# Optimization experiments

Hardware: AMD Instinct MI355X
Metric: run time of the kernel (lower is better)

## Reference

```python
import jax, jax.numpy as jnp
import numpy as np

BLOCK = 16
FP4_LEVELS = jnp.array([0.0, 0.5, 1.0, 1.5, 2.0, 3.0, 4.0, 6.0], dtype=jnp.float32)
FP4_MIDS = jnp.array([0.25, 0.75, 1.25, 1.75, 2.5, 3.5, 5.0], dtype=jnp.float32)
E4M3_MAX = 448.0
FP4_MAX = 6.0


def _fp4_round(v):
    # round-to-nearest onto signed E2M1 grid {0,.5,1,1.5,2,3,4,6}
    a = jnp.minimum(jnp.abs(v), FP4_MAX)
    idx = jnp.searchsorted(FP4_MIDS, a, side='right')
    return jnp.sign(v) * FP4_LEVELS[idx]


def _encode_scale(block_amax, global_amax):
    # two-level NVFP4 scaling: block scale stored as FP8 E4M3 relative to global scale
    g_scale = global_amax / (E4M3_MAX * FP4_MAX)
    s = block_amax / FP4_MAX
    s_q = jnp.clip(s / g_scale, 0.0, E4M3_MAX).astype(jnp.float8_e4m3fn).astype(jnp.float32) * g_scale
    return s_q


def nvfp4_qdq_1d(x, block=BLOCK):
    # blockwise fake-quant along the last dim (activations)
    sh = x.shape
    xb = x.reshape(sh[:-1] + (sh[-1] // block, block))
    g_amax = jnp.max(jnp.abs(x))
    b_amax = jnp.max(jnp.abs(xb), axis=-1, keepdims=True)
    s = _encode_scale(b_amax, g_amax)
    s_safe = jnp.where(s > 0, s, 1.0)
    dq = _fp4_round(xb / s_safe) * s
    return dq.reshape(sh)


def nvfp4_qdq_2d(w, block=BLOCK):
    # (16,16) 2D block fake-quant for the weight [out, in]
    O, I = w.shape
    wb = w.reshape(O // block, block, I // block, block)
    g_amax = jnp.max(jnp.abs(w))
    b_amax = jnp.max(jnp.abs(wb), axis=(1, 3), keepdims=True)
    s = _encode_scale(b_amax, g_amax)
    s_safe = jnp.where(s > 0, s, 1.0)
    dq = _fp4_round(wb / s_safe) * s
    return dq.reshape(O, I)


def setup_inputs() -> dict:
    key = jax.random.key(0)
    kx, kw = jax.random.split(key)
    B, S, D_IN, D_OUT = 4, 2048, 4096, 4096
    x = jax.random.normal(kx, (B, S, D_IN), dtype=jnp.float32)
    weight = jax.random.normal(kw, (D_OUT, D_IN), dtype=jnp.float32) * 0.02
    bias = jnp.zeros((D_OUT,), dtype=jnp.float32)
    return {"x": x, "weight": weight, "bias": bias}


def reference(x, weight, bias):
    x_hat = nvfp4_qdq_1d(x)
    x_ste = x + jax.lax.stop_gradient(x_hat - x)
    w_hat = nvfp4_qdq_2d(weight)
    w_ste = weight + jax.lax.stop_gradient(w_hat - weight)
    y = jnp.einsum('bsi,oi->bso', x_ste, w_ste)
    return y + bias
```

## Files before the change

### kernel.cpp

```cpp
#include <hip/hip_runtime.h>

typedef unsigned short u16;
typedef unsigned int u32;
typedef __bf16 bf16x8 __attribute__((ext_vector_type(8)));
typedef float f32x4 __attribute__((ext_vector_type(4)));


__device__ __forceinline__ float e4m3_rne(float r) {
  if (r < 0.015625f) {
    return rintf(r * 512.0f) * (1.0f / 512.0f);
  }
  u32 u = __float_as_uint(r);
  u32 lsb = (u >> 20) & 1u;
  u += 0x7FFFFu + lsb;
  u &= 0xFFF00000u;
  return __uint_as_float(u);
}

__device__ __forceinline__ float fp4_level(float a, const float* t) {
  return a < t[3] ? (a < t[1] ? (a < t[0] ? 0.0f : 0.5f)
                              : (a < t[2] ? 1.0f : 1.5f))
                  : (a < t[5] ? (a < t[4] ? 2.0f : 3.0f)
                              : (a < t[6] ? 4.0f : 6.0f));
}

__device__ __forceinline__ void gload_lds16(const u16* g, void* l) {
  __builtin_amdgcn_global_load_lds(
      (const __attribute__((address_space(1))) void*)g,
      (__attribute__((address_space(3))) void*)l, 16, 0, 0);
}


__global__ void __launch_bounds__(256) amax_part_kernel(const float4* __restrict__ p,
                                                        int n4, float* __restrict__ part) {
  float m = 0.0f;
  int stride = gridDim.x * 256;
  for (int i = blockIdx.x * 256 + threadIdx.x; i < n4; i += stride) {
    float4 v = p[i];
    m = fmaxf(m, fmaxf(fmaxf(fabsf(v.x), fabsf(v.y)), fmaxf(fabsf(v.z), fabsf(v.w))));
  }
#pragma unroll
  for (int o = 32; o > 0; o >>= 1) m = fmaxf(m, __shfl_xor(m, o));
  __shared__ float red[4];
  int wid = threadIdx.x >> 6, lane = threadIdx.x & 63;
  if (lane == 0) red[wid] = m;
  __syncthreads();
  if (threadIdx.x == 0)
    part[blockIdx.x] = fmaxf(fmaxf(red[0], red[1]), fmaxf(red[2], red[3]));
}

__global__ void __launch_bounds__(256) finalize_kernel(const float* __restrict__ px,
                                                       const float* __restrict__ pw,
                                                       float* __restrict__ scal,
                                                       int nx, int nw) {
  int tid = threadIdx.x;
  float mx = 0.0f, mw = 0.0f;
  for (int i = tid; i < nx; i += 256) mx = fmaxf(mx, px[i]);
  for (int i = tid; i < nw; i += 256) mw = fmaxf(mw, pw[i]);
#pragma unroll
  for (int o = 32; o > 0; o >>= 1) {
    mx = fmaxf(mx, __shfl_xor(mx, o));
    mw = fmaxf(mw, __shfl_xor(mw, o));
  }
  __shared__ float rx[4], rw[4];
  int wid = tid >> 6, lane = tid & 63;
  if (lane == 0) { rx[wid] = mx; rw[wid] = mw; }
  __syncthreads();
  if (tid == 0) {
    scal[0] = fmaxf(fmaxf(rx[0], rx[1]), fmaxf(rx[2], rx[3]));
    scal[1] = fmaxf(fmaxf(rw[0], rw[1]), fmaxf(rw[2], rw[3]));
  }
}


__global__ void __launch_bounds__(256) quant_x_kernel(const float* __restrict__ x,
                                                      const float* __restrict__ scal,
                                                      u16* __restrict__ q, int nblk) {
  int b = blockIdx.x * 256 + threadIdx.x;
  if (b >= nblk) return;
  const float4* px = (const float4*)(x + (size_t)b * 16);
  float4 v[4];
  v[0] = px[0]; v[1] = px[1]; v[2] = px[2]; v[3] = px[3];
  float am = 0.0f;
  const float* vf = (const float*)v;
#pragma unroll
  for (int i = 0; i < 16; ++i) am = fmaxf(am, fabsf(vf[i]));

  float g = scal[0] / 2688.0f;
  float ratio = fminf(fmaxf((am / 6.0f) / g, 0.0f), 448.0f);
  float sq = e4m3_rne(ratio);
  float s = sq * g;
  float ss = s > 0.0f ? s : 1.0f;
  float t[7] = {0.25f * ss, 0.75f * ss, 1.25f * ss, 1.75f * ss,
                2.5f * ss, 3.5f * ss, 5.0f * ss};

  union { u16 h[16]; uint4 v4[2]; } ou;
#pragma unroll
  for (int i = 0; i < 16; ++i) {
    float qv = copysignf(fp4_level(fabsf(vf[i]), t) * sq, vf[i]);
    ou.h[i] = (u16)(__float_as_uint(qv) >> 16);
  }
  uint4* qd = (uint4*)(q + (size_t)b * 16);
  qd[0] = ou.v4[0];
  qd[1] = ou.v4[1];
}


__global__ void __launch_bounds__(256) quant_w_kernel(const float* __restrict__ w,
                                                      const float* __restrict__ scal,
                                                      u16* __restrict__ q, int ntc, int K) {
  int wav = blockIdx.x * 4 + (threadIdx.x >> 6);
  int lane = threadIdx.x & 63;
  int tr = wav / ntc, tc = wav % ntc;
  int r = lane >> 2, c = (lane & 3) * 4;
  size_t off = (size_t)(tr * 16 + r) * K + tc * 16 + c;
  float4 v = *(const float4*)(w + off);
  float am = fmaxf(fmaxf(fabsf(v.x), fabsf(v.y)), fmaxf(fabsf(v.z), fabsf(v.w)));
#pragma unroll
  for (int o = 32; o > 0; o >>= 1) am = fmaxf(am, __shfl_xor(am, o));

  float g = scal[1] / 2688.0f;
  float ratio = fminf(fmaxf((am / 6.0f) / g, 0.0f), 448.0f);
  float sq = e4m3_rne(ratio);
  float s = sq * g;
  float ss = s > 0.0f ? s : 1.0f;
  float t[7] = {0.25f * ss, 0.75f * ss, 1.25f * ss, 1.75f * ss,
                2.5f * ss, 3.5f * ss, 5.0f * ss};

  float vf[4] = {v.x, v.y, v.z, v.w};
  union { u16 h[4]; uint2 v2; } ou;
#pragma unroll
  for (int i = 0; i < 4; ++i) {
    float qv = copysignf(fp4_level(fabsf(vf[i]), t) * sq, vf[i]);
    ou.h[i] = (u16)(__float_as_uint(qv) >> 16);
  }
  *(uint2*)(q + off) = ou.v2;
}


#define BM 256
#define BN 256
#define BK 64

__global__ void __launch_bounds__(512, 2) gemm_kernel(const u16* __restrict__ A,
                                                      const u16* __restrict__ B,
                                                      const float* __restrict__ bias,
                                                      const float* __restrict__ scal,
                                                      float* __restrict__ out,
                                                      int M, int N, int K) {
  extern __shared__ char lds[];
  const int tid = threadIdx.x;
  const int wid = tid >> 6, lane = tid & 63;
  const int fr = lane & 15, fc = lane >> 4;
  const int wm = wid >> 2, wn = wid & 3;
  const int sw = (fr & 7) << 4;

  int nwg = gridDim.x, bid = blockIdx.x;
  int q8 = nwg >> 3, r8 = nwg & 7;
  int xcd = bid & 7, loc = bid >> 3;
  int wg = (xcd < r8 ? xcd * (q8 + 1) : r8 * (q8 + 1) + (xcd - r8) * q8) + loc;
  int ntn = N / BN;
  int tm = wg / ntn, tn = wg % ntn;
  int brow = tm * BM, bcol = tn * BN;

  const int srow = tid >> 3;
  const int scol = ((((tid & 7) << 4) ^ ((srow & 7) << 4)) >> 1);
  const u16* gA = A + (size_t)(brow + srow) * K + scol;
  const u16* gB = B + (size_t)(bcol + srow) * K + scol;
  const size_t K64r = (size_t)K * 64;
  const int ldsOff = wid << 10;

#define STAGE_A4(buf, kt) do {                                                \
    gload_lds16(gA + (kt), (buf) + ldsOff);                                   \
    gload_lds16(gA + K64r + (kt), (buf) + 8192 + ldsOff);                     \
    gload_lds16(gA + 2 * K64r + (kt), (buf) + 16384 + ldsOff);                \
    gload_lds16(gA + 3 * K64r + (kt), (buf) + 24576 + ldsOff);                \
  } while (0)
#define STAGE_B4(buf, kt) do {                                                \
    gload_lds16(gB + (kt), (buf) + 32768 + ldsOff);                           \
    gload_lds16(gB + K64r + (kt), (buf) + 40960 + ldsOff);                    \
    gload_lds16(gB + 2 * K64r + (kt), (buf) + 49152 + ldsOff);                \
    gload_lds16(gB + 3 * K64r + (kt), (buf) + 57344 + ldsOff);                \
  } while (0)

  const u32 ldsbase = (u32)(uintptr_t)(__attribute__((address_space(3))) char*)lds;
  const u32 cb0 = (u32)((fc << 4) ^ sw);
  const u32 cb1 = cb0 ^ 64u;
  const u32 aB0 = ldsbase + (u32)((wm * 128 + fr) * 128) + cb0;
  const u32 aB1 = ldsbase + (u32)((wm * 128 + fr) * 128) + cb1;
  const u32 bB0 = ldsbase + 32768u + (u32)((wn * 64 + fr) * 128) + cb0;
  const u32 bB1 = ldsbase + 32768u + (u32)((wn * 64 + fr) * 128) + cb1;

#define DSR(dst, ad, off) \
  asm volatile("ds_read_b128 %0, %1 offset:" off : "=v"(dst) : "v"(ad))

#define LOAD_A0(dst) do { \
  DSR(dst[0][0], aC0, "0");    DSR(dst[0][1], aC1, "0");    \
  DSR(dst[1][0], aC0, "2048"); DSR(dst[1][1], aC1, "2048"); \
  DSR(dst[2][0], aC0, "4096"); DSR(dst[2][1], aC1, "4096"); \
  DSR(dst[3][0], aC0, "6144"); DSR(dst[3][1], aC1, "6144"); } while (0)
#define LOAD_A1(dst) do { \
  DSR(dst[0][0], aC0, "8192");  DSR(dst[0][1], aC1, "8192");  \
  DSR(dst[1][0], aC0, "10240"); DSR(dst[1][1], aC1, "10240"); \
  DSR(dst[2][0], aC0, "12288"); DSR(dst[2][1], aC1, "12288"); \
  DSR(dst[3][0], aC0, "14336"); DSR(dst[3][1], aC1, "14336"); } while (0)
#define LOAD_B0() do { \
  DSR(b0[0][0], bC0, "0");    DSR(b0[0][1], bC1, "0");    \
  DSR(b0[1][0], bC0, "2048"); DSR(b0[1][1], bC1, "2048"); } while (0)
#define LOAD_B1() do { \
  DSR(b1[0][0], bC0, "4096"); DSR(b1[0][1], bC1, "4096"); \
  DSR(b1[1][0], bC0, "6144"); DSR(b1[1][1], bC1, "6144"); } while (0)

#define MMA(qm, qn, af, bf)                                                  \
  _Pragma("unroll") for (int j_ = 0; j_ < 4; ++j_)                           \
  _Pragma("unroll") for (int n_ = 0; n_ < 2; ++n_)                           \
  _Pragma("unroll") for (int k_ = 0; k_ < 2; ++k_)                           \
    acc[(qm) * 4 + j_][(qn) * 2 + n_] = __builtin_amdgcn_mfma_f32_16x16x32_bf16( \
        af[j_][k_], bf[n_][k_], acc[(qm) * 4 + j_][(qn) * 2 + n_], 0, 0, 0);

#define WAITK(n)                                             \
  asm volatile("s_waitcnt lgkmcnt(" #n ")" ::: "memory");    \
  __builtin_amdgcn_sched_barrier(0);

  f32x4 acc[8][4];
  f32x4 zero = {0.0f, 0.0f, 0.0f, 0.0f};
#pragma unroll
  for (int m = 0; m < 8; ++m)
#pragma unroll
    for (int n = 0; n < 4; ++n) acc[m][n] = zero;

  const int NT = K / BK;

  STAGE_A4(lds, 0);
  STAGE_B4(lds, 0);
  asm volatile("s_waitcnt vmcnt(0)" ::: "memory");
  __builtin_amdgcn_s_barrier();

  bf16x8 a[4][2], a2[4][2], b0[2][2], b1[2][2];
  int cur = 0;
  for (int t = 0; t < NT; ++t) {
    const u32 bo = (u32)(cur << 16);
    const u32 aC0 = aB0 + bo, aC1 = aB1 + bo;
    const u32 bC0 = bB0 + bo, bC1 = bB1 + bo;
    char* bq = lds + (cur ^ 1) * 65536;
    const int kt1 = (t + 1) * BK;
    const int st1 = (t + 1 < NT);

    LOAD_A0(a);
    LOAD_B0();
    LOAD_B1();
    LOAD_A1(a2);
    if (st1) { STAGE_A4(bq, kt1); STAGE_B4(bq, kt1); }

    WAITK(12);
    __builtin_amdgcn_s_setprio(1);
    MMA(0, 0, a, b0);
    __builtin_amdgcn_s_setprio(0);
    WAITK(8);
    __builtin_amdgcn_s_setprio(1);
    MMA(0, 1, a, b1);
    __builtin_amdgcn_s_setprio(0);
    WAITK(0);
    __builtin_amdgcn_s_setprio(1);
    MMA(1, 1, a2, b1);
    MMA(1, 0, a2, b0);
    __builtin_amdgcn_s_setprio(0);

    asm volatile("s_waitcnt vmcnt(0)" ::: "memory");
    __builtin_amdgcn_s_barrier();
    __builtin_amdgcn_sched_barrier(0);
    cur ^= 1;
  }

  float gs = (scal[0] / 2688.0f) * (scal[1] / 2688.0f);
#pragma unroll
  for (int n = 0; n < 4; ++n) {
    int col = bcol + wn * 64 + n * 16 + fr;
    float bv = bias[col];
#pragma unroll
    for (int m = 0; m < 8; ++m) {
      int row0 = brow + wm * 128 + m * 16 + (fc << 2);
      f32x4 v = acc[m][n];
#pragma unroll
      for (int j = 0; j < 4; ++j)
        out[(size_t)(row0 + j) * N + col] = v[j] * gs + bv;
    }
  }
}


extern "C" void kernel_launch(void* const* d_in, const int* in_sizes, int n_in,
                              void* d_out, int out_size, void* d_ws, size_t ws_size,
                              hipStream_t stream) {
  const float* x = (const float*)d_in[0];
  const float* w = (const float*)d_in[1];
  const float* bias = (const float*)d_in[2];
  float* out = (float*)d_out;

  const int DOUT = in_sizes[2];
  const int K = in_sizes[1] / DOUT;
  const int M = in_sizes[0] / K;
  const int N = DOUT;

  float* scal = (float*)d_ws;
  float* px = (float*)((char*)d_ws + 256);
  float* pw = px + 1024;
  u16* qw = (u16*)((char*)d_ws + 8192);
  u16* qx = (u16*)((char*)d_ws + 8192 + (size_t)N * K * 2);

  amax_part_kernel<<<1024, 256, 0, stream>>>((const float4*)x, (M * K) / 4, px);
  amax_part_kernel<<<512, 256, 0, stream>>>((const float4*)w, (N * K) / 4, pw);
  finalize_kernel<<<1, 256, 0, stream>>>(px, pw, scal, 1024, 512);

  int nblk = (M * K) / 16;
  quant_x_kernel<<<(nblk + 255) / 256, 256, 0, stream>>>(x, scal, qx, nblk);

  int ntiles = (N / 16) * (K / 16);
  quant_w_kernel<<<ntiles / 4, 256, 0, stream>>>(w, scal, qw, K / 16, K);

  gemm_kernel<<<(M / BM) * (N / BN), 512, 131072, stream>>>(qx, qw, bias, scal, out,
                                                            M, N, K);
}
```

Baseline: 336.6 us.

## Switch GEMM inner loop to 32x32x16 MFMA with four pipelined K-slices

Replaces the 16x16x32 bf16 MFMA tiling with 32x32x16 MFMA instructions. Each wave now covers its 128x64 tile with 4x2 accumulators of 16 floats. The K=64 tile is split into four 16-wide slices whose LDS reads are double-buffered against the MFMAs of the previous slice. The aim is fewer MFMA issues and fewer LDS reads per FLOP, at the cost of a new swizzle and epilogue mapping that must match the stored layout.

```diff
diff --git a/kernel.cpp b/kernel.cpp
--- a/kernel.cpp
+++ b/kernel.cpp
@@ -4,6 +4,7 @@
 typedef unsigned int u32;
 typedef __bf16 bf16x8 __attribute__((ext_vector_type(8)));
 typedef float f32x4 __attribute__((ext_vector_type(4)));
+typedef float f32x16 __attribute__((ext_vector_type(16)));
 
 
 __device__ __forceinline__ float e4m3_rne(float r) {
@@ -151,9 +152,8 @@
   extern __shared__ char lds[];
   const int tid = threadIdx.x;
   const int wid = tid >> 6, lane = tid & 63;
-  const int fr = lane & 15, fc = lane >> 4;
+  const int l31 = lane & 31, fc2 = lane >> 5;
   const int wm = wid >> 2, wn = wid & 3;
-  const int sw = (fr & 7) << 4;
 
   int nwg = gridDim.x, bid = blockIdx.x;
   int q8 = nwg >> 3, r8 = nwg & 7;
@@ -184,50 +184,42 @@
   } while (0)
 
   const u32 ldsbase = (u32)(uintptr_t)(__attribute__((address_space(3))) char*)lds;
-  const u32 cb0 = (u32)((fc << 4) ^ sw);
-  const u32 cb1 = cb0 ^ 64u;
-  const u32 aB0 = ldsbase + (u32)((wm * 128 + fr) * 128) + cb0;
-  const u32 aB1 = ldsbase + (u32)((wm * 128 + fr) * 128) + cb1;
-  const u32 bB0 = ldsbase + 32768u + (u32)((wn * 64 + fr) * 128) + cb0;
-  const u32 bB1 = ldsbase + 32768u + (u32)((wn * 64 + fr) * 128) + cb1;
+  const u32 cbase = ((u32)(fc2 << 4)) ^ ((u32)((lane & 7) << 4));
+  const u32 aRow = ldsbase + (u32)((wm * 128 + l31) * 128);
+  const u32 bRow = ldsbase + 32768u + (u32)((wn * 64 + l31) * 128);
+  const u32 aC0 = aRow + (cbase ^ 0u),  aC1 = aRow + (cbase ^ 32u);
+  const u32 aC2 = aRow + (cbase ^ 64u), aC3 = aRow + (cbase ^ 96u);
+  const u32 bC0 = bRow + (cbase ^ 0u),  bC1 = bRow + (cbase ^ 32u);
+  const u32 bC2 = bRow + (cbase ^ 64u), bC3 = bRow + (cbase ^ 96u);
 
 #define DSR(dst, ad, off) \
   asm volatile("ds_read_b128 %0, %1 offset:" off : "=v"(dst) : "v"(ad))
 
-#define LOAD_A0(dst) do { \
-  DSR(dst[0][0], aC0, "0");    DSR(dst[0][1], aC1, "0");    \
-  DSR(dst[1][0], aC0, "2048"); DSR(dst[1][1], aC1, "2048"); \
-  DSR(dst[2][0], aC0, "4096"); DSR(dst[2][1], aC1, "4096"); \
-  DSR(dst[3][0], aC0, "6144"); DSR(dst[3][1], aC1, "6144"); } while (0)
-#define LOAD_A1(dst) do { \
-  DSR(dst[0][0], aC0, "8192");  DSR(dst[0][1], aC1, "8192");  \
-  DSR(dst[1][0], aC0, "10240"); DSR(dst[1][1], aC1, "10240"); \
-  DSR(dst[2][0], aC0, "12288"); DSR(dst[2][1], aC1, "12288"); \
-  DSR(dst[3][0], aC0, "14336"); DSR(dst[3][1], aC1, "14336"); } while (0)
-#define LOAD_B0() do { \
-  DSR(b0[0][0], bC0, "0");    DSR(b0[0][1], bC1, "0");    \
-  DSR(b0[1][0], bC0, "2048"); DSR(b0[1][1], bC1, "2048"); } while (0)
-#define LOAD_B1() do { \
-  DSR(b1[0][0], bC0, "4096"); DSR(b1[0][1], bC1, "4096"); \
-  DSR(b1[1][0], bC0, "6144"); DSR(b1[1][1], bC1, "6144"); } while (0)
-
-#define MMA(qm, qn, af, bf)                                                  \
-  _Pragma("unroll") for (int j_ = 0; j_ < 4; ++j_)                           \
-  _Pragma("unroll") for (int n_ = 0; n_ < 2; ++n_)                           \
-  _Pragma("unroll") for (int k_ = 0; k_ < 2; ++k_)                           \
-    acc[(qm) * 4 + j_][(qn) * 2 + n_] = __builtin_amdgcn_mfma_f32_16x16x32_bf16( \
-        af[j_][k_], bf[n_][k_], acc[(qm) * 4 + j_][(qn) * 2 + n_], 0, 0, 0);
+#define SLICE_READ(ak, bk, A_, B_) do {                                       \
+    DSR(A_[0], ak, "0");    DSR(A_[1], ak, "4096");                           \
+    DSR(A_[2], ak, "8192"); DSR(A_[3], ak, "12288");                          \
+    DSR(B_[0], bk, "0");    DSR(B_[1], bk, "4096");                           \
+  } while (0)
+
+#define MMA_SLICE(A_, B_)                                                     \
+  _Pragma("unroll") for (int mt_ = 0; mt_ < 4; ++mt_)                         \
+  _Pragma("unroll") for (int nt_ = 0; nt_ < 2; ++nt_)                         \
+    acc[mt_][nt_] = __builtin_amdgcn_mfma_f32_32x32x16_bf16(                  \
+        A_[mt_], B_[nt_], acc[mt_][nt_], 0, 0, 0);
 
 #define WAITK(n)                                             \
   asm volatile("s_waitcnt lgkmcnt(" #n ")" ::: "memory");    \
   __builtin_amdgcn_sched_barrier(0);
-
-  f32x4 acc[8][4];
-  f32x4 zero = {0.0f, 0.0f, 0.0f, 0.0f};
-#pragma unroll
-  for (int m = 0; m < 8; ++m)
-#pragma unroll
-    for (int n = 0; n < 4; ++n) acc[m][n] = zero;
+#define PR1 __builtin_amdgcn_s_setprio(1)
+#define PR0 __builtin_amdgcn_s_setprio(0)
+
+  f32x16 acc[4][2];
+#pragma unroll
+  for (int m = 0; m < 4; ++m)
+#pragma unroll
+    for (int n = 0; n < 2; ++n)
+#pragma unroll
+      for (int e = 0; e < 16; ++e) acc[m][n][e] = 0.0f;
 
   const int NT = K / BK;
 
@@ -236,35 +228,30 @@
   asm volatile("s_waitcnt vmcnt(0)" ::: "memory");
   __builtin_amdgcn_s_barrier();
 
-  bf16x8 a[4][2], a2[4][2], b0[2][2], b1[2][2];
+  bf16x8 aP[4], bP[2], aQ[4], bQ[2];
   int cur = 0;
   for (int t = 0; t < NT; ++t) {
     const u32 bo = (u32)(cur << 16);
-    const u32 aC0 = aB0 + bo, aC1 = aB1 + bo;
-    const u32 bC0 = bB0 + bo, bC1 = bB1 + bo;
+    const u32 aT0 = aC0 + bo, aT1 = aC1 + bo, aT2 = aC2 + bo, aT3 = aC3 + bo;
+    const u32 bT0 = bC0 + bo, bT1 = bC1 + bo, bT2 = bC2 + bo, bT3 = bC3 + bo;
     char* bq = lds + (cur ^ 1) * 65536;
     const int kt1 = (t + 1) * BK;
     const int st1 = (t + 1 < NT);
 
-    LOAD_A0(a);
-    LOAD_B0();
-    LOAD_B1();
-    LOAD_A1(a2);
+    SLICE_READ(aT0, bT0, aP, bP);
     if (st1) { STAGE_A4(bq, kt1); STAGE_B4(bq, kt1); }
 
-    WAITK(12);
-    __builtin_amdgcn_s_setprio(1);
-    MMA(0, 0, a, b0);
-    __builtin_amdgcn_s_setprio(0);
-    WAITK(8);
-    __builtin_amdgcn_s_setprio(1);
-    MMA(0, 1, a, b1);
-    __builtin_amdgcn_s_setprio(0);
+    SLICE_READ(aT1, bT1, aQ, bQ);
+    WAITK(6);
+    PR1; MMA_SLICE(aP, bP); PR0;
+    SLICE_READ(aT2, bT2, aP, bP);
+    WAITK(6);
+    PR1; MMA_SLICE(aQ, bQ); PR0;
+    SLICE_READ(aT3, bT3, aQ, bQ);
+    WAITK(6);
+    PR1; MMA_SLICE(aP, bP); PR0;
     WAITK(0);
-    __builtin_amdgcn_s_setprio(1);
-    MMA(1, 1, a2, b1);
-    MMA(1, 0, a2, b0);
-    __builtin_amdgcn_s_setprio(0);
+    PR1; MMA_SLICE(aQ, bQ); PR0;
 
     asm volatile("s_waitcnt vmcnt(0)" ::: "memory");
     __builtin_amdgcn_s_barrier();
@@ -274,16 +261,16 @@
 
   float gs = (scal[0] / 2688.0f) * (scal[1] / 2688.0f);
 #pragma unroll
-  for (int n = 0; n < 4; ++n) {
-    int col = bcol + wn * 64 + n * 16 + fr;
+  for (int nt = 0; nt < 2; ++nt) {
+    int col = bcol + wn * 64 + nt * 32 + l31;
     float bv = bias[col];
 #pragma unroll
-    for (int m = 0; m < 8; ++m) {
-      int row0 = brow + wm * 128 + m * 16 + (fc << 2);
-      f32x4 v = acc[m][n];
-#pragma unroll
-      for (int j = 0; j < 4; ++j)
-        out[(size_t)(row0 + j) * N + col] = v[j] * gs + bv;
+    for (int mt = 0; mt < 4; ++mt) {
+      f32x16 v = acc[mt][nt];
+      int rb = brow + wm * 128 + mt * 32 + fc2 * 4;
+#pragma unroll
+      for (int r = 0; r < 16; ++r)
+        out[(size_t)(rb + (r & 3) + 8 * (r >> 2)) * N + col] = v[r] * gs + bv;
     }
   }
 }
```

After: 349.9 us. +3.9%, slower.
